# Optimization experiments

Measured on AMD Instinct MI355X. Metric: run time of the kernel, lower is better.

The kernel has to match this reference:

```python
import jax, jax.numpy as jnp
import numpy as np
from jax import lax

N_NODES = 50000
N_EDGES = 200000
N_FEAT = 512
HIDDEN = 256
N_FILT = 4
FIND_STEPS = 18  # > log2(N_NODES); valid because union-by-size bounds tree height


def _find(parent, x):
    # pointer-jump to root; fixed trip count, root is a fixed point (parent[r]==r)
    return lax.fori_loop(0, FIND_STEPS, lambda i, y: parent[y], x)


def persistence_dim0(v, src, dst):
    """Dim-0 persistence diagram for one filtration.
    v: (N,) node filtration values. src/dst: (E,) int32 edge endpoints.
    Returns (N, 2) array of (birth, death) pairs, one per node.
    Union-find over edges sorted by filtration value max(v[u], v[w]);
    when two components merge, the younger one's minimum node dies at the edge value.
    Essential components die at max(v). The scan is purely integer-typed so the
    only differentiable path to deaths is the final gather from edge weights w.
    """
    N = v.shape[0]
    w = jnp.maximum(v[src], v[dst])  # (E,) edge filtration values
    edge_order = lax.stop_gradient(jnp.argsort(w)).astype(jnp.int32)
    vertex_order = jnp.argsort(lax.stop_gradient(v))
    rank = jnp.zeros((N,), jnp.int32).at[vertex_order].set(jnp.arange(N, dtype=jnp.int32))

    init = (
        jnp.arange(N, dtype=jnp.int32),      # parent
        jnp.ones((N,), jnp.int32),           # component size (union by size)
        rank,                                 # min birth-rank of component, stored at root
        jnp.arange(N, dtype=jnp.int32),      # node achieving min rank, stored at root
        jnp.full((N,), -1, jnp.int32),       # killing edge index per node (-1 = essential)
    )

    def step(carry, e):
        parent, size, mrank, mnode, kill = carry
        u = src[e]
        t = dst[e]
        ru = _find(parent, u)
        rt = _find(parent, t)
        merge = ru != rt
        # younger component = larger min birth-rank; its representative node dies here
        ru_young = mrank[ru] > mrank[rt]
        young = jnp.where(ru_young, ru, rt)
        kn = mnode[young]
        kill = kill.at[kn].set(jnp.where(merge, e, kill[kn]))
        # union by size: attach smaller tree under larger
        big = jnp.where(size[ru] >= size[rt], ru, rt)
        small = jnp.where(size[ru] >= size[rt], rt, ru)
        parent = parent.at[small].set(jnp.where(merge, big, parent[small]))
        size = size.at[big].set(jnp.where(merge, size[ru] + size[rt], size[big]))
        nm_rank = jnp.minimum(mrank[ru], mrank[rt])
        nm_node = jnp.where(mrank[ru] <= mrank[rt], mnode[ru], mnode[rt])
        mrank = mrank.at[big].set(jnp.where(merge, nm_rank, mrank[big]))
        mnode = mnode.at[big].set(jnp.where(merge, nm_node, mnode[big]))
        return (parent, size, mrank, mnode, kill), None

    (_, _, _, _, kill), _ = lax.scan(step, init, edge_order)
    death = jnp.where(kill >= 0, w[jnp.maximum(kill, 0)], jnp.max(v))
    return jnp.stack([v, death], axis=-1)  # (N, 2)


def setup_inputs() -> dict:
    key = jax.random.key(0)
    k1, k2, k3, k4 = jax.random.split(key, 4)
    X = jax.random.normal(k1, (N_NODES, N_FEAT), dtype=jnp.float32)
    edge_index = jax.random.randint(k2, (2, N_EDGES), 0, N_NODES, dtype=jnp.int64)
    s1 = 1.0 / np.sqrt(N_FEAT)
    s2 = 1.0 / np.sqrt(HIDDEN)
    W1 = jax.random.uniform(k3, (N_FEAT, HIDDEN), jnp.float32, -s1, s1)
    b1 = jnp.zeros((HIDDEN,), jnp.float32)
    W2 = jax.random.uniform(k4, (HIDDEN, N_FILT), jnp.float32, -s2, s2)
    b2 = jnp.zeros((N_FILT,), jnp.float32)
    return {"X": X, "W1": W1, "b1": b1, "W2": W2, "b2": b2, "edge_index": edge_index}


def reference(X, W1, b1, W2, b2, edge_index):
    # filtration MLP: Linear -> ReLU -> Linear, (n_nodes, n_filtrations)
    filt = jax.nn.relu(X @ W1 + b1) @ W2 + b2
    src = edge_index[0].astype(jnp.int32)
    dst = edge_index[1].astype(jnp.int32)
    # (n_filtrations, n_nodes, 2) dim-0 persistence diagrams
    diagrams = jax.vmap(lambda v: persistence_dim0(v, src, dst))(filt.T)
    return diagrams
```

## Files before the change

### kernel.cpp

```cpp
#include <hip/hip_runtime.h>
#include <stdint.h>

#define NN 50000
#define NE 200000
#define NFEAT 512
#define NHID 256
#define NPART 32
#define NBLKE 196
#define NBLKN 49

typedef unsigned long long u64;
typedef unsigned int u32;
typedef unsigned short u16;

__device__ const int PB[NPART + 1] = {
    0, 12288, 23936, 35008, 45568, 55616, 65152, 74240, 82880,
    91072, 98880, 106304, 113344, 120064, 126464, 132544, 138304,
    143808, 148992, 153920, 158656, 163136, 167424, 171456, 175296,
    178944, 182464, 185792, 188928, 191936, 194816, 197504, 200000};

__device__ __forceinline__ u32 encf(float x) {
  u32 u = __float_as_uint(x);
  return (u & 0x80000000u) ? ~u : (u | 0x80000000u);
}
__device__ __forceinline__ float decf(u32 y) {
  u32 u = (y & 0x80000000u) ? (y ^ 0x80000000u) : ~y;
  return __uint_as_float(u);
}

#define SWZ(c) ((c) ^ ((((c) >> 5) & 7) << 2))

__global__ __launch_bounds__(256) void mlp_kernel(
    const float* __restrict__ X, const float* __restrict__ W1,
    const float* __restrict__ b1, const float* __restrict__ W2,
    const float* __restrict__ b2, float* __restrict__ filt)
{
  __shared__ float As[64][33];
  __shared__ float Ws[32][256];
  __shared__ float W2s[256][4];

  const int tid = threadIdx.x;
  const int row0 = blockIdx.x * 64;
  const int tr = tid >> 4, tc = tid & 15;

  for (int i = tid; i < NHID * 4; i += 256) W2s[i >> 2][i & 3] = W2[i];

  float4 acc[4][4];
  #pragma unroll
  for (int i = 0; i < 4; i++)
    #pragma unroll
    for (int q = 0; q < 4; q++) acc[i][q] = make_float4(0.f, 0.f, 0.f, 0.f);

  for (int k0 = 0; k0 < NFEAT; k0 += 32) {
    __syncthreads();
    {
      const int r = tid >> 3, c4 = (tid & 7) << 2;
      #pragma unroll
      for (int rr = 0; rr < 2; rr++) {
        const int row = r + rr * 32;
        const int grow = row0 + row;
        float4 v = make_float4(0.f, 0.f, 0.f, 0.f);
        if (grow < NN) v = *(const float4*)&X[(size_t)grow * NFEAT + k0 + c4];
        As[row][c4 + 0] = v.x; As[row][c4 + 1] = v.y;
        As[row][c4 + 2] = v.z; As[row][c4 + 3] = v.w;
      }
      const int wr = tid >> 6, wc4 = (tid & 63) << 2;
      const int pc = SWZ(wc4);
      #pragma unroll
      for (int rr = 0; rr < 8; rr++) {
        const int rowk = wr + rr * 4;
        float4 v = *(const float4*)&W1[(size_t)(k0 + rowk) * NHID + wc4];
        *(float4*)&Ws[rowk][pc] = v;
      }
    }
    __syncthreads();
    #pragma unroll 8
    for (int kk = 0; kk < 32; kk++) {
      const float a0 = As[tr * 4 + 0][kk], a1 = As[tr * 4 + 1][kk],
                  a2 = As[tr * 4 + 2][kk], a3 = As[tr * 4 + 3][kk];
      #pragma unroll
      for (int q = 0; q < 4; q++) {
        const int col = tc * 16 + q * 4;
        const float4 wv = *(const float4*)&Ws[kk][SWZ(col)];
        acc[0][q].x += a0 * wv.x; acc[0][q].y += a0 * wv.y;
        acc[0][q].z += a0 * wv.z; acc[0][q].w += a0 * wv.w;
        acc[1][q].x += a1 * wv.x; acc[1][q].y += a1 * wv.y;
        acc[1][q].z += a1 * wv.z; acc[1][q].w += a1 * wv.w;
        acc[2][q].x += a2 * wv.x; acc[2][q].y += a2 * wv.y;
        acc[2][q].z += a2 * wv.z; acc[2][q].w += a2 * wv.w;
        acc[3][q].x += a3 * wv.x; acc[3][q].y += a3 * wv.y;
        acc[3][q].w += a3 * wv.w; acc[3][q].z += a3 * wv.z;
      }
    }
  }

  float p[4][4];
  #pragma unroll
  for (int i = 0; i < 4; i++)
    #pragma unroll
    for (int f = 0; f < 4; f++) p[i][f] = 0.f;

  #pragma unroll
  for (int q = 0; q < 4; q++) {
    const int colb = tc * 16 + q * 4;
    float bb[4];
    #pragma unroll
    for (int j = 0; j < 4; j++) bb[j] = b1[colb + j];
    #pragma unroll
    for (int i = 0; i < 4; i++) {
      float h[4] = {acc[i][q].x + bb[0], acc[i][q].y + bb[1],
                    acc[i][q].z + bb[2], acc[i][q].w + bb[3]};
      #pragma unroll
      for (int j = 0; j < 4; j++) {
        const float hh = fmaxf(h[j], 0.f);
        #pragma unroll
        for (int f = 0; f < 4; f++) p[i][f] += hh * W2s[colb + j][f];
      }
    }
  }

  #pragma unroll
  for (int m = 1; m < 16; m <<= 1)
    #pragma unroll
    for (int i = 0; i < 4; i++)
      #pragma unroll
      for (int f = 0; f < 4; f++)
        p[i][f] += __shfl_xor(p[i][f], m, 64);

  if (tc == 0) {
    const float c0 = b2[0], c1 = b2[1], c2 = b2[2], c3 = b2[3];
    #pragma unroll
    for (int i = 0; i < 4; i++) {
      const int row = row0 + tr * 4 + i;
      if (row < NN) {
        float4 o = make_float4(p[i][0] + c0, p[i][1] + c1, p[i][2] + c2, p[i][3] + c3);
        *(float4*)&filt[(size_t)row * 4] = o;
      }
    }
  }
}

__global__ void zero4_kernel(u32* __restrict__ maxv) {
  if (threadIdx.x < 4) maxv[threadIdx.x] = 0u;
}

__global__ __launch_bounds__(256) void maxv_kernel(const float* __restrict__ filt,
                                                   u32* __restrict__ maxv)
{
  __shared__ u32 lm[4];
  if (threadIdx.x < 4) lm[threadIdx.x] = 0u;
  __syncthreads();
  const int n = blockIdx.x * 256 + threadIdx.x;
  if (n < NN) {
    const float4 v = *(const float4*)&filt[(size_t)n * 4];
    atomicMax(&lm[0], encf(v.x));
    atomicMax(&lm[1], encf(v.y));
    atomicMax(&lm[2], encf(v.z));
    atomicMax(&lm[3], encf(v.w));
  }
  __syncthreads();
  if (threadIdx.x < 4) atomicMax(&maxv[threadIdx.x], lm[threadIdx.x]);
}

__global__ __launch_bounds__(256) void nodeprep_kernel(const float* __restrict__ filt,
                                                       u64* __restrict__ nodekeys)
{
  const int n = blockIdx.x * 256 + threadIdx.x;
  const int f = blockIdx.y;
  if (n < NN) {
    const float v = filt[(size_t)n * 4 + f];
    nodekeys[(size_t)f * NN + n] = ((u64)encf(v) << 32) | (u32)n;
  }
}

__global__ __launch_bounds__(256) void radix_hist(
    const u64* __restrict__ src, u32* __restrict__ hist, int n, int nblk, int shift)
{
  __shared__ u32 cnt[256];
  const int tid = threadIdx.x;
  const int blk = blockIdx.x;
  const int f = blockIdx.y;
  src += (size_t)f * n;
  hist += (size_t)f * 256 * nblk;
  cnt[tid] = 0;
  __syncthreads();
  #pragma unroll
  for (int k = 0; k < 4; k++) {
    const int i = blk * 1024 + k * 256 + tid;
    if (i < n) atomicAdd(&cnt[(u32)(src[i] >> shift) & 255u], 1u);
  }
  __syncthreads();
  hist[(size_t)tid * nblk + blk] = cnt[tid];
}

__global__ __launch_bounds__(256) void radix_scan_rows(
    u32* __restrict__ hist, u32* __restrict__ rowtot, int nblk)
{
  __shared__ u32 buf[256];
  const int d = blockIdx.x, f = blockIdx.y;
  const int tid = threadIdx.x;
  u32* row = hist + ((size_t)f * 256 + d) * nblk;
  u32 v = (tid < nblk) ? row[tid] : 0u;
  buf[tid] = v;
  __syncthreads();
  for (int off = 1; off < 256; off <<= 1) {
    const u32 t = (tid >= off) ? buf[tid - off] : 0u;
    __syncthreads();
    buf[tid] += t;
    __syncthreads();
  }
  if (tid < nblk) row[tid] = buf[tid] - v;
  if (tid == 255) rowtot[f * 256 + d] = buf[255];
}

__global__ __launch_bounds__(256) void radix_scan_digits(u32* __restrict__ rowtot)
{
  __shared__ u32 buf[256];
  const int f = blockIdx.x, tid = threadIdx.x;
  const u32 v = rowtot[f * 256 + tid];
  buf[tid] = v;
  __syncthreads();
  for (int off = 1; off < 256; off <<= 1) {
    const u32 t = (tid >= off) ? buf[tid - off] : 0u;
    __syncthreads();
    buf[tid] += t;
    __syncthreads();
  }
  rowtot[f * 256 + tid] = buf[tid] - v;
}

__global__ __launch_bounds__(256) void radix_scatter(
    const u64* __restrict__ src, u64* __restrict__ dst,
    const u32* __restrict__ hist, const u32* __restrict__ rowtot,
    int n, int nblk, int shift)
{
  __shared__ u32 baseD[256];
  __shared__ u32 accum[256];
  __shared__ u32 roundCnt[4 * 256];
  const int tid = threadIdx.x;
  const int blk = blockIdx.x;
  const int f = blockIdx.y;
  const int lane = tid & 63, wid = tid >> 6;
  src += (size_t)f * n;
  dst += (size_t)f * n;
  baseD[tid] = hist[(size_t)f * 256 * nblk + (size_t)tid * nblk + blk] +
               rowtot[f * 256 + tid];
  accum[tid] = 0;
  for (int k = 0; k < 4; k++) {
    roundCnt[tid] = 0; roundCnt[tid + 256] = 0;
    roundCnt[tid + 512] = 0; roundCnt[tid + 768] = 0;
    __syncthreads();
    const int i = blk * 1024 + k * 256 + tid;
    const bool valid = (i < n);
    const u64 key = valid ? src[i] : 0ull;
    const u32 d = (u32)(key >> shift) & 255u;
    u64 peers = __ballot(valid);
    #pragma unroll
    for (int b = 0; b < 8; b++) {
      const u64 bal = __ballot((d >> b) & 1u);
      peers &= ((d >> b) & 1u) ? bal : ~bal;
    }
    const u32 rank = (u32)__popcll(peers & ((1ull << lane) - 1ull));
    if (valid && (__ffsll((long long)peers) - 1 == lane))
      roundCnt[wid * 256 + d] = (u32)__popcll(peers);
    __syncthreads();
    if (valid) {
      u32 off = baseD[d] + accum[d] + rank;
      for (int w2 = 0; w2 < wid; w2++) off += roundCnt[w2 * 256 + d];
      dst[off] = key;
    }
    __syncthreads();
    accum[tid] += roundCnt[tid] + roundCnt[256 + tid] +
                  roundCnt[512 + tid] + roundCnt[768 + tid];
    __syncthreads();
  }
}

__global__ __launch_bounds__(256) void rank_kernel(const u64* __restrict__ nodekeys,
                                                   u32* __restrict__ rankOf,
                                                   u32* __restrict__ nodeOf)
{
  const int j = blockIdx.x * 256 + threadIdx.x;
  const int f = blockIdx.y;
  if (j < NN) {
    const u64 kk = nodekeys[(size_t)f * NN + j];
    const u32 node = (u32)(kk & 0xffffffffu);
    rankOf[(size_t)f * NN + node] = (u32)j;
    nodeOf[(size_t)f * NN + j] = node;
  }
}

__global__ __launch_bounds__(256) void init_kernel(
    const float* __restrict__ filt, const u32* __restrict__ maxv,
    float* __restrict__ out)
{
  const int n = blockIdx.x * 256 + threadIdx.x;
  const int f = blockIdx.y;
  if (n < NN) {
    const size_t idx = (size_t)f * NN + n;
    out[idx * 2 + 0] = filt[(size_t)n * 4 + f];
    out[idx * 2 + 1] = decf(maxv[f]);
  }
}

__global__ __launch_bounds__(256) void prep_kernel(
    const int* __restrict__ ei, const float* __restrict__ filt,
    const u32* __restrict__ rankOf, u64* __restrict__ pairs)
{
  const int e = blockIdx.x * 256 + threadIdx.x;
  if (e >= NE) return;
  const int s = ei[e];
  const int d = ei[NE + e];
  const float4 vs = *(const float4*)&filt[(size_t)s * 4];
  const float4 vd = *(const float4*)&filt[(size_t)d * 4];
  float wf[4] = {fmaxf(vs.x, vd.x), fmaxf(vs.y, vd.y),
                 fmaxf(vs.z, vd.z), fmaxf(vs.w, vd.w)};
  #pragma unroll
  for (int f = 0; f < 4; f++) {
    const u32 ru = rankOf[(size_t)f * NN + s];
    const u32 rt = rankOf[(size_t)f * NN + d];
    pairs[(size_t)f * NE + e] = ((u64)encf(wf[f]) << 32) | ((ru << 16) | rt);
  }
}

__global__ __launch_bounds__(1024) void uf_kernel(
    const u64* __restrict__ pairs, u64* __restrict__ qbuf, u32* __restrict__ qcnt)
{
  __shared__ __align__(16) u16 par[NN];
  __shared__ __align__(16) u32 scratch[1024];
  const int q = blockIdx.x, f = blockIdx.y;
  const int tid = threadIdx.x;
  const u64* ps = pairs + (size_t)f * NE;
  const int lo = PB[q], hi = PB[q + 1];

  u32* par32 = (u32*)par;
  for (int j = tid; j < NN / 2; j += 1024)
    par32[j] = ((u32)(2 * j + 1) << 16) | (u32)(2 * j);
  __syncthreads();

  {
    volatile u16* vpar = par;
    for (int e = tid; e < lo; e += 1024) {
      const u32 pr = (u32)(ps[e] & 0xffffffffu);
      u32 x = pr >> 16, y = pr & 0xffffu;
      while (true) {
        u32 px = vpar[x];
        while (px != x) { const u32 g = vpar[px]; vpar[x] = (u16)g; x = g; px = vpar[x]; }
        u32 py = vpar[y];
        while (py != y) { const u32 g = vpar[py]; vpar[y] = (u16)g; y = g; py = vpar[y]; }
        if (x == y) break;
        const u32 h = (x > y) ? x : y;
        const u32 l = x ^ y ^ h;
        volatile u32* w32 = (volatile u32*)par32 + (h >> 1);
        const bool hiH = (h & 1u) != 0u;
        bool hooked = false, lost = false;
        while (!hooked && !lost) {
          const u32 cur = *w32;
          const u32 half = hiH ? (cur >> 16) : (cur & 0xffffu);
          if (half != h) { lost = true; break; }
          const u32 nw = hiH ? ((cur & 0x0000ffffu) | (l << 16))
                             : ((cur & 0xffff0000u) | l);
          if (atomicCAS((u32*)w32, cur, nw) == cur) hooked = true;
        }
        if (hooked) break;
        x = h; y = l;
      }
    }
  }
  __syncthreads();

  if (tid >= 64) return;
  const int lane = tid;
  u64* qb = qbuf + (size_t)f * NE + lo;
  u32 qcount = 0;
  uint4* h4 = (uint4*)scratch;
  const uint4 zz = make_uint4(0u, 0u, 0u, 0u);

  u64 pair0 = ps[lo + lane];
  u64 pair1 = (lo + 64 < hi) ? ps[lo + 64 + lane] : 0ull;

  for (int base = lo; base < hi; base += 64) {
    u64 pair2 = 0ull;
    if (base + 128 < hi) pair2 = ps[base + 128 + lane];

    const u32 pr = (u32)(pair0 & 0xffffffffu);
    const u32 deathw = (u32)(pair0 >> 32);
    const int u = (int)(pr >> 16), t = (int)(pr & 0xffffu);

    int ru = u, rt = t;
    u32 pu = par[ru], pt = par[rt];
    while (pu != (u32)ru || pt != (u32)rt) {
      const u32 gu = par[pu];
      const u32 gt = par[pt];
      if (pu != (u32)ru) { par[ru] = (u16)gu; ru = (int)gu; }
      if (pt != (u32)rt) { par[rt] = (u16)gt; rt = (int)gt; }
      pu = par[ru]; pt = par[rt];
    }

    const bool mg = (ru != rt);
    const u32 winv = (ru < rt) ? (u32)ru : (u32)rt;
    const u32 losev = (u32)(ru ^ rt) ^ winv;
    const u64 mball = __ballot(mg);
    const int nm = (int)__popcll(mball);

    bool flag = false;
    if (nm > 1) {
      #pragma unroll
      for (int k = 0; k < 4; k++) h4[lane + 64 * k] = zz;
      const u32 hu = ((u32)ru * 2654435761u) >> 22;
      const u32 ht = ((u32)rt * 2654435761u) >> 22;
      if (mg) { atomicAdd(&scratch[hu], 1u); atomicAdd(&scratch[ht], 1u); }
      asm volatile("s_waitcnt lgkmcnt(0)" ::: "memory");
      u32 cl = 0u;
      if (mg) cl = scratch[(losev == (u32)ru) ? hu : ht];
      flag = mg && (cl >= 2u);
    }

    u32 myLose = 0xffffffffu, myWin = 0u;
    if (mg && !flag) { myLose = losev; myWin = winv; }

    u64 chain = __ballot(flag);
    u32 mp = ((u32)ru << 16) | (u32)rt;
    while (chain) {
      const int l = __ffsll((long long)chain) - 1;
      chain &= (chain - 1);
      const u32 ab = (u32)__builtin_amdgcn_readlane((int)mp, l);
      const u32 a = ab >> 16, b = ab & 0xffffu;
      if (a != b) {
        const u32 win = a < b ? a : b;
        const u32 lose = a ^ b ^ win;
        const bool isme = (lane == l);
        myLose = isme ? lose : myLose;
        myWin = isme ? win : myWin;
        const u32 h2 = mp >> 16, l2m = mp & 0xffffu;
        mp = ((h2 == lose ? win : h2) << 16) | (l2m == lose ? win : l2m);
      }
    }

    const u64 mmask = __ballot(myLose != 0xffffffffu);
    if (myLose != 0xffffffffu) {
      par[myLose] = (u16)myWin;
      const u32 idx = (u32)__popcll(mmask & ((1ull << lane) - 1ull));
      qb[qcount + idx] = ((u64)deathw << 32) | myLose;
    }
    qcount += (u32)__popcll(mmask);

    asm volatile("s_waitcnt lgkmcnt(0)" ::: "memory");
    __builtin_amdgcn_sched_barrier(0);
    pair0 = pair1; pair1 = pair2;
  }
  if (lane == 0) qcnt[f * NPART + q] = qcount;
}

__global__ __launch_bounds__(256) void finalize_kernel(
    const u64* __restrict__ qbuf, const u32* __restrict__ qcnt,
    const u32* __restrict__ nodeOf, float* __restrict__ out)
{
  const int e = blockIdx.x * 256 + threadIdx.x;
  const int f = blockIdx.y;
  if (e >= NE) return;
  int q = 0;
  while (q < NPART - 1 && e >= PB[q + 1]) q++;
  if ((u32)(e - PB[q]) < qcnt[f * NPART + q]) {
    const u64 v = qbuf[(size_t)f * NE + e];
    const u32 lose = (u32)(v & 0xffffffffu);
    const u32 node = nodeOf[(size_t)f * NN + lose];
    out[((size_t)f * NN + node) * 2 + 1] = decf((u32)(v >> 32));
  }
}

extern "C" void kernel_launch(void* const* d_in, const int* in_sizes, int n_in,
                              void* d_out, int out_size, void* d_ws, size_t ws_size,
                              hipStream_t stream)
{
  const float* X  = (const float*)d_in[0];
  const float* W1 = (const float*)d_in[1];
  const float* b1 = (const float*)d_in[2];
  const float* W2 = (const float*)d_in[3];
  const float* b2 = (const float*)d_in[4];
  const int*   EI = (const int*)d_in[5];
  float* out = (float*)d_out;

  char* w = (char*)d_ws;
  u64*  A      = (u64*)w;   w += (size_t)4 * NE * sizeof(u64);
  char* Bb     = w;         w += (size_t)4 * NE * sizeof(u64);
  u64*  qbuf   = (u64*)w;   w += (size_t)4 * NE * sizeof(u64);
  float* filt  = (float*)w; w += (size_t)NN * 4 * sizeof(float);
  u32*  rankOf = (u32*)w;   w += (size_t)4 * NN * sizeof(u32);
  u32*  nodeOf = (u32*)w;   w += (size_t)4 * NN * sizeof(u32);
  u32*  qcnt   = (u32*)w;   w += 128 * sizeof(u32);
  u32*  rowtot = (u32*)w;   w += 4 * 256 * sizeof(u32);
  u32*  maxv   = (u32*)w;   w += 4 * sizeof(u32);

  u64* NA   = (u64*)Bb;
  u64* NB   = (u64*)(Bb + 1600000);
  u64* EB   = (u64*)Bb;
  u32* nhist = rankOf;
  u32* ehist = (u32*)filt;

  const size_t need = (size_t)(w - (char*)d_ws);
  if (ws_size < need) return;

  const int nodeBlocks = (NN + 255) / 256;
  const int edgeBlocks = (NE + 255) / 256;

  zero4_kernel<<<dim3(1), dim3(64), 0, stream>>>(maxv);
  mlp_kernel<<<dim3((NN + 63) / 64), dim3(256), 0, stream>>>(X, W1, b1, W2, b2, filt);
  maxv_kernel<<<dim3(nodeBlocks, 1), dim3(256), 0, stream>>>(filt, maxv);
  nodeprep_kernel<<<dim3(nodeBlocks, 4), dim3(256), 0, stream>>>(filt, NA);

  {
    u64 *s = NA, *d = NB;
    for (int p = 0; p < 4; p++) {
      const int sh = 32 + 8 * p;
      radix_hist<<<dim3(NBLKN, 4), dim3(256), 0, stream>>>(s, nhist, NN, NBLKN, sh);
      radix_scan_rows<<<dim3(256, 4), dim3(256), 0, stream>>>(nhist, rowtot, NBLKN);
      radix_scan_digits<<<dim3(4), dim3(256), 0, stream>>>(rowtot);
      radix_scatter<<<dim3(NBLKN, 4), dim3(256), 0, stream>>>(s, d, nhist, rowtot,
                                                              NN, NBLKN, sh);
      u64* t = s; s = d; d = t;
    }
  }

  rank_kernel<<<dim3(nodeBlocks, 4), dim3(256), 0, stream>>>(NA, rankOf, nodeOf);
  init_kernel<<<dim3(nodeBlocks, 4), dim3(256), 0, stream>>>(filt, maxv, out);
  prep_kernel<<<dim3(edgeBlocks, 1), dim3(256), 0, stream>>>(EI, filt, rankOf, A);

  {
    u64 *s = A, *d = EB;
    for (int p = 0; p < 4; p++) {
      const int sh = 32 + 8 * p;
      radix_hist<<<dim3(NBLKE, 4), dim3(256), 0, stream>>>(s, ehist, NE, NBLKE, sh);
      radix_scan_rows<<<dim3(256, 4), dim3(256), 0, stream>>>(ehist, rowtot, NBLKE);
      radix_scan_digits<<<dim3(4), dim3(256), 0, stream>>>(rowtot);
      radix_scatter<<<dim3(NBLKE, 4), dim3(256), 0, stream>>>(s, d, ehist, rowtot,
                                                              NE, NBLKE, sh);
      u64* t = s; s = d; d = t;
    }
  }

  uf_kernel<<<dim3(NPART, 4), dim3(1024), 0, stream>>>(A, qbuf, qcnt);

  finalize_kernel<<<dim3(edgeBlocks, 4), dim3(256), 0, stream>>>(qbuf, qcnt, nodeOf, out);
}
```

Baseline: 1.172 ms.

## Rebalance union-find partitions, flatten prefix union loop, add periodic path-compression sweeps

Repartitions the sorted edge list into 28 partitions with larger early chunks, so fewer blocks each replay a long prefix. The prefix union-find loop becomes a single wavefront-uniform loop that interleaves both finds and the CAS hook one step at a time, which cuts lane divergence from nested while loops. After every 16K-edge chunk, all threads fully compress parent pointers to roots, keeping later finds short. The cost is extra block-wide barriers and full-array sweeps, and the partition sizes become less balanced.

```diff
diff --git a/kernel.cpp b/kernel.cpp
--- a/kernel.cpp
+++ b/kernel.cpp
@@ -5,7 +5,8 @@
 #define NE 200000
 #define NFEAT 512
 #define NHID 256
-#define NPART 32
+#define NPART 28
+#define SWEEPCH 16384
 #define NBLKE 196
 #define NBLKN 49
 
@@ -14,10 +15,10 @@
 typedef unsigned short u16;
 
 __device__ const int PB[NPART + 1] = {
-    0, 12288, 23936, 35008, 45568, 55616, 65152, 74240, 82880,
-    91072, 98880, 106304, 113344, 120064, 126464, 132544, 138304,
-    143808, 148992, 153920, 158656, 163136, 167424, 171456, 175296,
-    178944, 182464, 185792, 188928, 191936, 194816, 197504, 200000};
+    0, 21376, 40640, 57984, 73600, 87616, 100288, 111680, 121920,
+    131136, 139456, 146944, 153664, 159744, 165184, 170112, 174528,
+    178496, 182080, 185280, 188160, 190784, 193152, 195264, 197184,
+    198912, 199488, 199808, 200000};
 
 __device__ __forceinline__ u32 encf(float x) {
   u32 u = __float_as_uint(x);
@@ -340,31 +341,46 @@
 
   {
     volatile u16* vpar = par;
-    for (int e = tid; e < lo; e += 1024) {
-      const u32 pr = (u32)(ps[e] & 0xffffffffu);
-      u32 x = pr >> 16, y = pr & 0xffffu;
-      while (true) {
-        u32 px = vpar[x];
-        while (px != x) { const u32 g = vpar[px]; vpar[x] = (u16)g; x = g; px = vpar[x]; }
-        u32 py = vpar[y];
-        while (py != y) { const u32 g = vpar[py]; vpar[y] = (u16)g; y = g; py = vpar[y]; }
-        if (x == y) break;
-        const u32 h = (x > y) ? x : y;
-        const u32 l = x ^ y ^ h;
-        volatile u32* w32 = (volatile u32*)par32 + (h >> 1);
-        const bool hiH = (h & 1u) != 0u;
-        bool hooked = false, lost = false;
-        while (!hooked && !lost) {
-          const u32 cur = *w32;
-          const u32 half = hiH ? (cur >> 16) : (cur & 0xffffu);
-          if (half != h) { lost = true; break; }
-          const u32 nw = hiH ? ((cur & 0x0000ffffu) | (l << 16))
-                             : ((cur & 0xffff0000u) | l);
-          if (atomicCAS((u32*)w32, cur, nw) == cur) hooked = true;
+    for (int chunk = 0; chunk < lo; chunk += SWEEPCH) {
+      int cend = chunk + SWEEPCH; if (cend > lo) cend = lo;
+      for (int e = chunk + tid; e < cend; e += 1024) {
+        const u32 pr = (u32)(ps[e] & 0xffffffffu);
+        u32 x = pr >> 16, y = pr & 0xffffu;
+        bool pend = true;
+        while (__any(pend)) {
+          if (pend) {
+            const u32 px = vpar[x];
+            const u32 py = vpar[y];
+            const bool xr = (px == x), yr = (py == y);
+            if (!xr) { const u32 g = vpar[px]; vpar[x] = (u16)g; x = g; }
+            if (!yr) { const u32 g = vpar[py]; vpar[y] = (u16)g; y = g; }
+            if (xr && yr) {
+              if (x == y) pend = false;
+              else {
+                const u32 h = (x > y) ? x : y;
+                const u32 l = x ^ y ^ h;
+                volatile u32* w32 = (volatile u32*)par32 + (h >> 1);
+                const u32 cur = *w32;
+                const bool hiH = (h & 1u) != 0u;
+                if ((hiH ? (cur >> 16) : (cur & 0xffffu)) == h) {
+                  const u32 nw = hiH ? ((cur & 0x0000ffffu) | (l << 16))
+                                     : ((cur & 0xffff0000u) | l);
+                  if (atomicCAS((u32*)w32, cur, nw) == cur) pend = false;
+                }
+                x = h; y = l;
+              }
+            }
+          }
         }
-        if (hooked) break;
-        x = h; y = l;
-      }
+      }
+      __syncthreads();
+      for (int x0 = tid; x0 < NN; x0 += 1024) {
+        u32 p = par[x0];
+        u32 g = par[p];
+        while (g != p) { p = g; g = par[p]; }
+        par[x0] = (u16)p;
+      }
+      __syncthreads();
     }
   }
   __syncthreads();
```

Measured after the change: 1.885 ms. 1.61x slower.

## Precompute prefix union-find checkpoints in global memory to shorten per-partition replay

Applied to the files above, without the earlier changes.

Adds a global-memory concurrent union-find pass that builds connectivity snapshots at fixed edge-prefix checkpoints (every CSTEP edges), spread across many blocks per checkpoint. Each uf_kernel block then loads the nearest checkpoint instead of rebuilding connectivity from edge 0, so it only replays edges from that checkpoint up to its partition start. The partition bounds are rebalanced to equal sizes, since replay cost no longer grows with position. The cost is an extra init kernel, redundant prefix union work across 7 checkpoints, and global atomics. The gpar buffer aliases the radix scratch region, which is safe only if that region is no longer needed by then.

```diff
diff --git a/kernel.cpp b/kernel.cpp
--- a/kernel.cpp
+++ b/kernel.cpp
@@ -6,6 +6,9 @@
 #define NFEAT 512
 #define NHID 256
 #define NPART 32
+#define NCB 7
+#define CSTEP 25000
+#define NGUF 56
 #define NBLKE 196
 #define NBLKN 49
 
@@ -14,10 +17,12 @@
 typedef unsigned short u16;
 
 __device__ const int PB[NPART + 1] = {
-    0, 12288, 23936, 35008, 45568, 55616, 65152, 74240, 82880,
-    91072, 98880, 106304, 113344, 120064, 126464, 132544, 138304,
-    143808, 148992, 153920, 158656, 163136, 167424, 171456, 175296,
-    178944, 182464, 185792, 188928, 191936, 194816, 197504, 200000};
+    0, 6272, 12544, 18816, 25088, 31360, 37632, 43904, 50176,
+    56448, 62720, 68992, 75264, 81536, 87808, 94080, 100352,
+    106624, 112896, 119168, 125440, 131712, 137984, 144256, 150528,
+    156800, 163072, 169344, 175616, 181888, 188160, 194432, 200000};
+
+__device__ const int GOFF[NCB + 1] = {0, 2, 6, 12, 20, 30, 42, 56};
 
 __device__ __forceinline__ u32 encf(float x) {
   u32 u = __float_as_uint(x);
@@ -323,8 +328,49 @@
   }
 }
 
+__global__ __launch_bounds__(256) void gparinit_kernel(u32* __restrict__ gpar)
+{
+  const int n = blockIdx.x * 256 + threadIdx.x;
+  const int jf = blockIdx.y;
+  if (n < NN) gpar[(size_t)jf * NN + n] = (u32)n;
+}
+
+__global__ __launch_bounds__(1024) void guf_kernel(
+    const u64* __restrict__ pairs, u32* __restrict__ gpar)
+{
+  const int bx = blockIdx.x;
+  const int f = blockIdx.y;
+  int j = 0;
+  while (j < NCB - 1 && bx >= GOFF[j + 1]) j++;
+  const int b = bx - GOFF[j];
+  const int nb = 2 * (j + 1);
+  const int cb = CSTEP * (j + 1);
+  const int s0 = (int)(((long long)cb * b) / nb);
+  const int s1 = (int)(((long long)cb * (b + 1)) / nb);
+  u32* gp = gpar + (size_t)(j * 4 + f) * NN;
+  const u64* ps = pairs + (size_t)f * NE;
+
+  for (int e = s0 + (int)threadIdx.x; e < s1; e += 1024) {
+    const u32 pr = (u32)(ps[e] & 0xffffffffu);
+    u32 x = pr >> 16, y = pr & 0xffffu;
+    while (true) {
+      u32 px = gp[x];
+      while (px != x) { const u32 g = gp[px]; gp[x] = g; x = g; px = gp[x]; }
+      u32 py = gp[y];
+      while (py != y) { const u32 g = gp[py]; gp[y] = g; y = g; py = gp[y]; }
+      if (x == y) break;
+      const u32 h = (x > y) ? x : y;
+      const u32 l = x ^ y ^ h;
+      const u32 old = atomicCAS(&gp[h], h, l);
+      if (old == h) break;
+      x = old; y = l;
+    }
+  }
+}
+
 __global__ __launch_bounds__(1024) void uf_kernel(
-    const u64* __restrict__ pairs, u64* __restrict__ qbuf, u32* __restrict__ qcnt)
+    const u64* __restrict__ pairs, const u32* __restrict__ gpar,
+    u64* __restrict__ qbuf, u32* __restrict__ qcnt)
 {
   __shared__ __align__(16) u16 par[NN];
   __shared__ __align__(16) u32 scratch[1024];
@@ -332,15 +378,22 @@
   const int tid = threadIdx.x;
   const u64* ps = pairs + (size_t)f * NE;
   const int lo = PB[q], hi = PB[q + 1];
+  int jb = lo / CSTEP; if (jb > NCB) jb = NCB;
+  const int base = jb * CSTEP;
 
   u32* par32 = (u32*)par;
-  for (int j = tid; j < NN / 2; j += 1024)
-    par32[j] = ((u32)(2 * j + 1) << 16) | (u32)(2 * j);
+  if (jb == 0) {
+    for (int j = tid; j < NN / 2; j += 1024)
+      par32[j] = ((u32)(2 * j + 1) << 16) | (u32)(2 * j);
+  } else {
+    const u32* gp = gpar + (size_t)((jb - 1) * 4 + f) * NN;
+    for (int n = tid; n < NN; n += 1024) par[n] = (u16)gp[n];
+  }
   __syncthreads();
 
   {
     volatile u16* vpar = par;
-    for (int e = tid; e < lo; e += 1024) {
+    for (int e = base + tid; e < lo; e += 1024) {
       const u32 pr = (u32)(ps[e] & 0xffffffffu);
       u32 x = pr >> 16, y = pr & 0xffffu;
       while (true) {
@@ -379,9 +432,9 @@
   u64 pair0 = ps[lo + lane];
   u64 pair1 = (lo + 64 < hi) ? ps[lo + 64 + lane] : 0ull;
 
-  for (int base = lo; base < hi; base += 64) {
+  for (int base2 = lo; base2 < hi; base2 += 64) {
     u64 pair2 = 0ull;
-    if (base + 128 < hi) pair2 = ps[base + 128 + lane];
+    if (base2 + 128 < hi) pair2 = ps[base2 + 128 + lane];
 
     const u32 pr = (u32)(pair0 & 0xffffffffu);
     const u32 deathw = (u32)(pair0 >> 32);
@@ -495,6 +548,7 @@
   u64* NA   = (u64*)Bb;
   u64* NB   = (u64*)(Bb + 1600000);
   u64* EB   = (u64*)Bb;
+  u32* gpar = (u32*)Bb;
   u32* nhist = rankOf;
   u32* ehist = (u32*)filt;
 
@@ -539,7 +593,10 @@
     }
   }
 
-  uf_kernel<<<dim3(NPART, 4), dim3(1024), 0, stream>>>(A, qbuf, qcnt);
+  gparinit_kernel<<<dim3(nodeBlocks, NCB * 4), dim3(256), 0, stream>>>(gpar);
+  guf_kernel<<<dim3(NGUF, 4), dim3(1024), 0, stream>>>(A, gpar);
+
+  uf_kernel<<<dim3(NPART, 4), dim3(1024), 0, stream>>>(A, gpar, qbuf, qcnt);
 
   finalize_kernel<<<dim3(edgeBlocks, 4), dim3(256), 0, stream>>>(qbuf, qcnt, nodeOf, out);
 }
```

Result: slower. 1.259 ms (+7.4%).
